# Performance work log

Hardware: AMD Instinct MI355X
Metric: run time of the kernel (lower is better)

## Reference

```python
import jax, jax.numpy as jnp
import numpy as np

B, N, D_MODEL, H, D_FF, NB_FEAT = 2, 2048, 512, 8, 2048, 256
DH = D_MODEL // H


def layer_norm(x, g, b, eps=1e-5):
    mu = jnp.mean(x, axis=-1, keepdims=True)
    var = jnp.mean((x - mu) ** 2, axis=-1, keepdims=True)
    return g * (x - mu) / jnp.sqrt(var + eps) + b


def softmax_kernel(data, proj, is_query, eps=1e-4):
    # Performer FAVOR+ positive random features. data: [b,h,n,dh], proj: [m,dh]
    dn = data.shape[-1] ** -0.25
    ratio = proj.shape[0] ** -0.5
    dd = jnp.einsum('bhnd,jd->bhnj', dn * data, proj)
    diag = (jnp.sum(data ** 2, axis=-1, keepdims=True) * 0.5) * (dn ** 2)
    if is_query:
        m = jnp.max(dd, axis=-1, keepdims=True)
    else:
        m = jnp.max(dd)
    return ratio * (jnp.exp(dd - diag - m) + eps)


def setup_inputs() -> dict:
    key = jax.random.key(0)
    ks = jax.random.split(key, 12)
    sd = D_MODEL ** -0.5
    sf = D_FF ** -0.5
    return {
        'x': jax.random.normal(ks[0], (B, N, D_MODEL), jnp.float32),
        'Wq': jax.random.normal(ks[1], (D_MODEL, D_MODEL), jnp.float32) * sd,
        'bq': jnp.zeros((D_MODEL,), jnp.float32),
        'Wk': jax.random.normal(ks[2], (D_MODEL, D_MODEL), jnp.float32) * sd,
        'bk': jnp.zeros((D_MODEL,), jnp.float32),
        'Wv': jax.random.normal(ks[3], (D_MODEL, D_MODEL), jnp.float32) * sd,
        'bv': jnp.zeros((D_MODEL,), jnp.float32),
        'Wo': jax.random.normal(ks[4], (D_MODEL, D_MODEL), jnp.float32) * sd,
        'bo': jnp.zeros((D_MODEL,), jnp.float32),
        'proj': jax.random.normal(ks[5], (NB_FEAT, DH), jnp.float32),
        'W1': jax.random.normal(ks[6], (D_MODEL, D_FF), jnp.float32) * sd,
        'b1': jnp.zeros((D_FF,), jnp.float32),
        'W2': jax.random.normal(ks[7], (D_FF, D_MODEL), jnp.float32) * sf,
        'b2': jnp.zeros((D_MODEL,), jnp.float32),
        'g1': jnp.ones((D_MODEL,), jnp.float32),
        'beta1': jnp.zeros((D_MODEL,), jnp.float32),
        'g2': jnp.ones((D_MODEL,), jnp.float32),
        'beta2': jnp.zeros((D_MODEL,), jnp.float32),
    }


def reference(x, Wq, bq, Wk, bk, Wv, bv, Wo, bo, proj, W1, b1, W2, b2, g1, beta1, g2, beta2):
    b, n, d = x.shape
    heads = lambda W, bias: (x @ W + bias).reshape(b, n, H, DH).transpose(0, 2, 1, 3)  # bhnd
    q = softmax_kernel(heads(Wq, bq), proj, is_query=True)   # [b,h,n,m]
    k = softmax_kernel(heads(Wk, bk), proj, is_query=False)  # [b,h,n,m]
    v = heads(Wv, bv)                                        # [b,h,n,dh]
    # non-causal linear attention
    k_sum = jnp.sum(k, axis=-2)                                   # [b,h,m]
    D_inv = 1.0 / jnp.einsum('bhnf,bhf->bhn', q, k_sum)           # [b,h,n]
    context = jnp.einsum('bhnf,bhne->bhfe', k, v)                 # [b,h,m,dh]
    out = jnp.einsum('bhfe,bhnf,bhn->bhne', context, q, D_inv)    # [b,h,n,dh]
    # output_attentions=True: effective attention matrix (abs, head-mean, detached)
    attn = jnp.einsum('bhnf,bhmf->bhnm', q, k) * D_inv[..., None]
    attn_weight = jax.lax.stop_gradient(jnp.mean(jnp.abs(attn), axis=1))  # [b,n,n]
    out = out.transpose(0, 2, 1, 3).reshape(b, n, d)
    out = out @ Wo + bo
    # NOTE: original module has no residual connections
    h1 = layer_norm(out, g1, beta1)
    ff = jax.nn.relu(h1 @ W1 + b1) @ W2 + b2
    y = layer_norm(ff, g2, beta2)
    return y, attn_weight
```

## Files before the change

kernel.cpp:

```cpp
#include <hip/hip_runtime.h>
#include <math.h>

#define B_SZ   2
#define N_TOK  2048
#define DM     512
#define NH     8
#define DHH    64
#define NF     256
#define DFF    2048
#define HF     2048
#define LDQKV  1536

constexpr float DN_SCALE   = 0.35355339059327373f;
constexpr float DIAG_SCALE = 0.0625f;
constexpr float RATIO      = 0.0625f;
constexpr float FEPS       = 1e-4f;
constexpr float LN_EPS     = 1e-5f;

typedef __attribute__((ext_vector_type(8))) short bf16x8;
typedef __attribute__((ext_vector_type(8))) _Float16 f16x8;
typedef __attribute__((ext_vector_type(4))) float f32x4;

__device__ __forceinline__ short f2b(float f) {
  union { float f; unsigned u; } x; x.f = f;
  unsigned r = (x.u + 0x7fff + ((x.u >> 16) & 1)) >> 16;
  return (short)r;
}
__device__ __forceinline__ float b2f(short s) {
  union { unsigned u; float f; } x; x.u = ((unsigned)(unsigned short)s) << 16;
  return x.f;
}
__device__ __forceinline__ void gload16(const void* g, void* l) {
  __builtin_amdgcn_global_load_lds((const __attribute__((address_space(1))) void*)g,
                                   (__attribute__((address_space(3))) void*)l, 16, 0, 0);
}
__device__ __forceinline__ int swz64(int row, int kbyte) {
  return (row * 128 + kbyte) ^ ((row & 7) << 4);
}

constexpr size_t OFF_S0    = 0;
constexpr size_t OFF_CTXP  = 0;
constexpr size_t OFF_QB    = 4194304;
constexpr size_t OFF_OUT2  = 0;
constexpr size_t OFF_FF1B  = 2097152;
constexpr size_t OFF_FF2   = 6291456;
constexpr size_t OFF_QFB   = 8388608;
constexpr size_t OFF_KB    = 12582912;
constexpr size_t OFF_QKV   = 16777216;
constexpr size_t OFF_AOB   = 20971520;
constexpr size_t OFF_H1B   = 22020096;
constexpr size_t OFF_WOT   = 23068672;
constexpr size_t OFF_W1T   = 23199744;
constexpr size_t OFF_W2T   = 23724032;
constexpr size_t OFF_KSUM  = 24248320;
constexpr size_t OFF_DINV  = 24252416;
constexpr size_t OFF_CTXT  = 24285184;
constexpr size_t OFF_BMAX  = 24416256;
constexpr size_t OFF_GMAX  = 24416768;
constexpr size_t OFF_ROWC  = 24416832;
constexpr size_t OFF_PART  = 24420928;
constexpr size_t OFF_VSUMP = 24552000;

template<bool RELU, bool OUT_BF16, int BMODE, bool SWZ>
__global__ __launch_bounds__(256)
void gemm_mfma(const short* __restrict__ A, const short* __restrict__ Bt,
               const float* __restrict__ bias, void* __restrict__ Cout,
               int M, int N, int K, size_t sA, size_t sB, size_t sC, int ldC) {
  __shared__ short As[128 * 64];
  __shared__ short Bs[128 * 64];
  int tid = threadIdx.x;
  int lane = tid & 63, wave = tid >> 6;
  int wm = wave >> 1, wn = wave & 1;
  int bx = blockIdx.x, by = blockIdx.y;
  if (SWZ) {
    int nwg = gridDim.x * gridDim.y;
    int flat = by * gridDim.x + bx;
    int swz = (flat & 7) * (nwg >> 3) + (flat >> 3);
    bx = swz % gridDim.x; by = swz / gridDim.x;
  }
  int bm = by * 128, bn = bx * 128;
  const short* Ab = A + (size_t)blockIdx.z * sA;
  const short* Bb = Bt + (size_t)blockIdx.z * sB;
  const float* rc = (BMODE == 2) ? (bias + (size_t)blockIdx.z * M) : bias;

  f32x4 acc[4][4] = {};
  int srow = tid >> 3;
  int scol = (tid & 7) * 8;

  for (int k0 = 0; k0 < K; k0 += 64) {
    #pragma unroll
    for (int c = 0; c < 4; ++c) {
      int r = c * 32 + srow;
      gload16(Ab + (size_t)(bm + r) * K + k0 + scol, As + c * 2048 + wave * 512);
      gload16(Bb + (size_t)(bn + r) * K + k0 + scol, Bs + c * 2048 + wave * 512);
    }
    __syncthreads();
    #pragma unroll
    for (int kk = 0; kk < 2; ++kk) {
      bf16x8 af[4], bf[4];
      int kq = kk * 32 + (lane >> 4) * 8;
      #pragma unroll
      for (int i = 0; i < 4; ++i)
        af[i] = *(const bf16x8*)&As[(wm * 64 + i * 16 + (lane & 15)) * 64 + kq];
      #pragma unroll
      for (int j = 0; j < 4; ++j)
        bf[j] = *(const bf16x8*)&Bs[(wn * 64 + j * 16 + (lane & 15)) * 64 + kq];
      #pragma unroll
      for (int i = 0; i < 4; ++i)
        #pragma unroll
        for (int j = 0; j < 4; ++j)
          acc[i][j] = __builtin_amdgcn_mfma_f32_16x16x32_bf16(af[i], bf[j], acc[i][j], 0, 0, 0);
    }
    __syncthreads();
  }

  int row0 = bm + wm * 64, col0 = bn + wn * 64;
  #pragma unroll
  for (int i = 0; i < 4; ++i) {
    #pragma unroll
    for (int j = 0; j < 4; ++j) {
      int col = col0 + j * 16 + (lane & 15);
      float bv = (BMODE == 1) ? rc[col] : 0.f;
      #pragma unroll
      for (int r = 0; r < 4; ++r) {
        int row = row0 + i * 16 + (lane >> 4) * 4 + r;
        float v = acc[i][j][r] + bv;
        if (BMODE == 2) v += rc[row];
        if (RELU) v = fmaxf(v, 0.f);
        size_t off = (size_t)blockIdx.z * sC + (size_t)row * ldC + col;
        if (OUT_BF16) ((short*)Cout)[off] = f2b(v);
        else          ((float*)Cout)[off] = v;
      }
    }
  }
}

template<bool RELU, bool OUT_BF16>
__global__ __launch_bounds__(256)
void gemm_bn64(const short* __restrict__ A, const short* __restrict__ Bt,
               const float* __restrict__ bias, void* __restrict__ Cout,
               int M, int N, int K) {
  __shared__ short As[128 * 64];
  __shared__ short Bs[64 * 64];
  int tid = threadIdx.x, lane = tid & 63, wave = tid >> 6;
  int bn = blockIdx.x * 64, bm = blockIdx.y * 128;
  int srow = tid >> 3, scol = (tid & 7) * 8;
  f32x4 acc[2][4] = {};
  for (int k0 = 0; k0 < K; k0 += 64) {
    #pragma unroll
    for (int c = 0; c < 4; ++c)
      gload16(A + (size_t)(bm + c * 32 + srow) * K + k0 + scol, As + c * 2048 + wave * 512);
    #pragma unroll
    for (int c = 0; c < 2; ++c)
      gload16(Bt + (size_t)(bn + c * 32 + srow) * K + k0 + scol, Bs + c * 2048 + wave * 512);
    __syncthreads();
    #pragma unroll
    for (int kk = 0; kk < 2; ++kk) {
      bf16x8 af[2], bf[4];
      int kq = kk * 32 + (lane >> 4) * 8;
      #pragma unroll
      for (int i = 0; i < 2; ++i)
        af[i] = *(const bf16x8*)&As[(wave * 32 + i * 16 + (lane & 15)) * 64 + kq];
      #pragma unroll
      for (int j = 0; j < 4; ++j)
        bf[j] = *(const bf16x8*)&Bs[(j * 16 + (lane & 15)) * 64 + kq];
      #pragma unroll
      for (int i = 0; i < 2; ++i)
        #pragma unroll
        for (int j = 0; j < 4; ++j)
          acc[i][j] = __builtin_amdgcn_mfma_f32_16x16x32_bf16(af[i], bf[j], acc[i][j], 0, 0, 0);
    }
    __syncthreads();
  }
  #pragma unroll
  for (int i = 0; i < 2; ++i) {
    #pragma unroll
    for (int j = 0; j < 4; ++j) {
      int col = bn + j * 16 + (lane & 15);
      float bv = bias[col];
      #pragma unroll
      for (int r = 0; r < 4; ++r) {
        int row = bm + wave * 32 + i * 16 + (lane >> 4) * 4 + r;
        float v = acc[i][j][r] + bv;
        if (RELU) v = fmaxf(v, 0.f);
        if (OUT_BF16) ((short*)Cout)[(size_t)row * N + col] = f2b(v);
        else          ((float*)Cout)[(size_t)row * N + col] = v;
      }
    }
  }
}

__global__ void prep_kernel(const float* __restrict__ x, short* __restrict__ xb,
                            const float* Wq, const float* Wk, const float* Wv, const float* Wo,
                            short* Wqt, short* Wkt, short* Wvt, short* Wot,
                            const float* W1, short* W1t, const float* W2, short* W2t) {
  __shared__ float t[64][65];
  int id = blockIdx.x, tid = threadIdx.x;
  if (id >= 768) {
    size_t base = ((size_t)(id - 768) * 256 + tid) * 8;
    #pragma unroll
    for (int u = 0; u < 8; ++u) xb[base + u] = f2b(x[base + u]);
    return;
  }
  const float* W; short* Wt; int K, N, bx, by;
  if (id < 256) {
    int z = id >> 6, sub = id & 63;
    W  = (z == 0) ? Wq : (z == 1) ? Wk : (z == 2) ? Wv : Wo;
    Wt = (z == 0) ? Wqt : (z == 1) ? Wkt : (z == 2) ? Wvt : Wot;
    K = 512; N = 512; bx = sub & 7; by = sub >> 3;
  } else if (id < 512) {
    int sub = id - 256;
    W = W1; Wt = W1t; K = 512; N = 2048; bx = sub & 31; by = sub >> 5;
  } else {
    int sub = id - 512;
    W = W2; Wt = W2t; K = 2048; N = 512; bx = sub & 7; by = sub >> 3;
  }
  int k0 = by * 64, n0 = bx * 64;
  int lx = tid & 63, ly = tid >> 6;
  for (int r = ly; r < 64; r += 4)
    t[r][lx] = W[(size_t)(k0 + r) * N + n0 + lx];
  __syncthreads();
  for (int r = ly; r < 64; r += 4)
    Wt[(size_t)(n0 + r) * K + k0 + lx] = f2b(t[lx][r]);
}

template<bool IS_QUERY>
__global__ __launch_bounds__(256)
void feat_mfma_kernel(const float* __restrict__ qkv, int coff, const float* __restrict__ bias,
                      const float* __restrict__ proj, short* __restrict__ qout,
                      float* __restrict__ part, float* __restrict__ bmax) {
  __shared__ short qh[64 * 64], ql[64 * 64];
  __shared__ short ph[128 * 64], pl[128 * 64];
  __shared__ float dpart[64][4];
  __shared__ float diag[64];
  __shared__ float wred[4];
  __shared__ float colp[4][256];
  int t = threadIdx.x;
  int bh = blockIdx.y, b = bh >> 3, h = bh & 7;
  int n0 = blockIdx.x * 64;
  int lane = t & 63, w = t >> 6, l15 = lane & 15, lq = lane >> 4;

  {
    int r = t >> 2, cg = (t & 3) * 16;
    const float* src = qkv + (size_t)(b * N_TOK + n0 + r) * LDQKV + coff + h * 64 + cg;
    const float* bs = bias + h * 64 + cg;
    float ss = 0.f;
    #pragma unroll
    for (int c2 = 0; c2 < 2; ++c2) {
      f16x8 H, L;
      #pragma unroll
      for (int u = 0; u < 8; ++u) {
        float xv = src[c2 * 8 + u] + bs[c2 * 8 + u];
        ss += xv * xv;
        _Float16 hi = (_Float16)xv;
        H[u] = hi;
        L[u] = (_Float16)(xv - (float)hi);
      }
      int off = swz64(r, cg * 2 + c2 * 16);
      *(f16x8*)((char*)qh + off) = H;
      *(f16x8*)((char*)ql + off) = L;
    }
    dpart[r][t & 3] = ss;
  }
  __syncthreads();
  if (t < 64)
    diag[t] = (dpart[t][0] + dpart[t][1] + dpart[t][2] + dpart[t][3]) * DIAG_SCALE;

  f16x8 ah[2], al[2];
  #pragma unroll
  for (int kk = 0; kk < 2; ++kk) {
    int off = swz64(w * 16 + l15, kk * 64 + lq * 16);
    ah[kk] = *(f16x8*)((char*)qh + off);
    al[kk] = *(f16x8*)((char*)ql + off);
  }

  f32x4 acc[16] = {};
  #pragma unroll
  for (int half = 0; half < 2; ++half) {
    __syncthreads();
    {
      int r = t & 127, cg = (t >> 7) * 32;
      const float* src = proj + (size_t)(half * 128 + r) * DHH + cg;
      #pragma unroll
      for (int c2 = 0; c2 < 4; ++c2) {
        f16x8 H, L;
        #pragma unroll
        for (int u = 0; u < 8; ++u) {
          float xv = src[c2 * 8 + u];
          _Float16 hi = (_Float16)xv;
          H[u] = hi;
          L[u] = (_Float16)(xv - (float)hi);
        }
        int off = swz64(r, cg * 2 + c2 * 16);
        *(f16x8*)((char*)ph + off) = H;
        *(f16x8*)((char*)pl + off) = L;
      }
    }
    __syncthreads();
    #pragma unroll
    for (int jl = 0; jl < 8; ++jl) {
      int row = jl * 16 + l15;
      #pragma unroll
      for (int kk = 0; kk < 2; ++kk) {
        int off = swz64(row, kk * 64 + lq * 16);
        f16x8 bh8 = *(f16x8*)((char*)ph + off);
        f16x8 bl8 = *(f16x8*)((char*)pl + off);
        acc[half * 8 + jl] = __builtin_amdgcn_mfma_f32_16x16x32_f16(ah[kk], bh8, acc[half * 8 + jl], 0, 0, 0);
        acc[half * 8 + jl] = __builtin_amdgcn_mfma_f32_16x16x32_f16(al[kk], bh8, acc[half * 8 + jl], 0, 0, 0);
        acc[half * 8 + jl] = __builtin_amdgcn_mfma_f32_16x16x32_f16(ah[kk], bl8, acc[half * 8 + jl], 0, 0, 0);
      }
    }
  }

  if (IS_QUERY) {
    #pragma unroll
    for (int r = 0; r < 4; ++r) {
      float mx = -3.4e38f;
      #pragma unroll
      for (int j = 0; j < 16; ++j) mx = fmaxf(mx, acc[j][r]);
      #pragma unroll
      for (int o = 1; o < 16; o <<= 1) mx = fmaxf(mx, __shfl_xor(mx, o, 64));
      int lrow = w * 16 + lq * 4 + r;
      float dg = diag[lrow];
      float ddm = mx * DN_SCALE;
      size_t base = (size_t)(b * N_TOK + n0 + lrow) * HF + h * NF + l15;
      #pragma unroll
      for (int j = 0; j < 16; ++j) {
        float v = RATIO * (expf(acc[j][r] * DN_SCALE - dg - ddm) + FEPS);
        qout[base + j * 16] = f2b(v);
      }
    }
  } else {
    float mxall = -3.4e38f;
    float cs[16];
    #pragma unroll
    for (int j = 0; j < 16; ++j) cs[j] = 0.f;
    #pragma unroll
    for (int r = 0; r < 4; ++r) {
      int lrow = w * 16 + lq * 4 + r;
      float dg = diag[lrow];
      size_t base = (size_t)(b * N_TOK + n0 + lrow) * HF + h * NF + l15;
      #pragma unroll
      for (int j = 0; j < 16; ++j) {
        float a = acc[j][r];
        mxall = fmaxf(mxall, a);
        float e = expf(a * DN_SCALE - dg);
        cs[j] += e;
        qout[base + j * 16] = f2b(e);
      }
    }
    #pragma unroll
    for (int j = 0; j < 16; ++j) {
      cs[j] += __shfl_xor(cs[j], 16, 64);
      cs[j] += __shfl_xor(cs[j], 32, 64);
    }
    if (lq == 0) {
      #pragma unroll
      for (int j = 0; j < 16; ++j) colp[w][j * 16 + l15] = cs[j];
    }
    #pragma unroll
    for (int o = 1; o < 64; o <<= 1) mxall = fmaxf(mxall, __shfl_xor(mxall, o, 64));
    if (lane == 0) wred[w] = mxall;
    __syncthreads();
    part[(size_t)(bh * 32 + blockIdx.x) * 256 + t] =
        colp[0][t] + colp[1][t] + colp[2][t] + colp[3][t];
    if (t == 0)
      bmax[bh * 32 + blockIdx.x] =
          fmaxf(fmaxf(wred[0], wred[1]), fmaxf(wred[2], wred[3])) * DN_SCALE;
  }
}

__global__ void ksum_final_kernel(const float* __restrict__ part, const float* __restrict__ bmax,
                                  float* __restrict__ ksum, float* __restrict__ gmax) {
  __shared__ float red[4];
  __shared__ float bc[1];
  int bh = blockIdx.x, t = threadIdx.x;
  float m = fmaxf(bmax[t], bmax[t + 256]);
  #pragma unroll
  for (int o = 1; o < 64; o <<= 1) m = fmaxf(m, __shfl_xor(m, o, 64));
  if ((t & 63) == 0) red[t >> 6] = m;
  __syncthreads();
  if (t == 0) {
    bc[0] = fmaxf(fmaxf(red[0], red[1]), fmaxf(red[2], red[3]));
    if (bh == 0) gmax[0] = bc[0];
  }
  __syncthreads();
  float s = expf(-bc[0]);
  float sum = 0.f;
  #pragma unroll 8
  for (int c = 0; c < 32; ++c) sum += part[(size_t)(bh * 32 + c) * 256 + t];
  ksum[bh * 256 + t] = RATIO * (s * sum + (float)N_TOK * FEPS);
}

__global__ __launch_bounds__(256)
void dinvqs_kernel(const short* __restrict__ qfb, const float* __restrict__ ksum,
                   const float* __restrict__ gmax, float* __restrict__ Dinv,
                   float* __restrict__ rowc, short* __restrict__ qb) {
  __shared__ float wsum[4];
  int R = blockIdx.x;
  int b = R >> 11, n = R & 2047;
  int t = threadIdx.x;
  float sc = RATIO * expf(-gmax[0]);
  bf16x8 qv = *(const bf16x8*)(qfb + (size_t)R * HF + t * 8);
  const float* ks = ksum + b * 2048 + t * 8;
  float p = 0.f;
  #pragma unroll
  for (int u = 0; u < 8; ++u) p += b2f(qv[u]) * ks[u];
  #pragma unroll
  for (int o = 1; o < 32; o <<= 1) p += __shfl_xor(p, o, 64);
  float d = 1.0f / p;
  if ((t & 31) == 0) Dinv[(b * NH + (t >> 5)) * N_TOK + n] = d;
  float dv = d * 0.125f;
  float qs = 0.f;
  bf16x8 o8;
  #pragma unroll
  for (int u = 0; u < 8; ++u) {
    float qb_f = b2f(qv[u]) * dv;
    qs += qb_f;
    o8[u] = f2b(qb_f * sc);
  }
  *(bf16x8*)(qb + (size_t)R * HF + t * 8) = o8;
  #pragma unroll
  for (int o = 1; o < 64; o <<= 1) qs += __shfl_xor(qs, o, 64);
  if ((t & 63) == 0) wsum[t >> 6] = qs;
  __syncthreads();
  if (t == 0) rowc[R] = RATIO * FEPS * (wsum[0] + wsum[1] + wsum[2] + wsum[3]);
}

__global__ __launch_bounds__(256)
void ctx_part_kernel(const short* __restrict__ kb, const float* __restrict__ qkv,
                     const float* __restrict__ bv, float* __restrict__ ctxp,
                     float* __restrict__ vsump) {
  int bh = blockIdx.y, b = bh >> 3, h = bh & 7;
  int f0 = blockIdx.x * 64;
  int ns = blockIdx.z * 256;
  __shared__ float kf[32][68];
  __shared__ float vs[32][68];
  int tid = threadIdx.x;
  int tf = (tid >> 4) * 4, te = (tid & 15) * 4;
  float acc[4][4] = {};
  float vloc[4] = {};
  for (int n0 = ns; n0 < ns + 256; n0 += 32) {
    #pragma unroll
    for (int i = 0; i < 8; i++) {
      int idx = tid + i * 256;
      int nn = idx >> 6, f = idx & 63;
      kf[nn][f] = b2f(kb[(size_t)(b * N_TOK + n0 + nn) * HF + h * NF + f0 + f]);
    }
    #pragma unroll
    for (int i = 0; i < 8; i++) {
      int idx = tid + i * 256;
      int nn = idx >> 6, e = idx & 63;
      vs[nn][e] = qkv[(size_t)(b * N_TOK + n0 + nn) * LDQKV + 1024 + h * DHH + e] + bv[h * DHH + e];
    }
    __syncthreads();
    #pragma unroll
    for (int nn = 0; nn < 32; nn++) {
      float a[4], bb[4];
      #pragma unroll
      for (int i = 0; i < 4; i++) a[i] = kf[nn][tf + i];
      #pragma unroll
      for (int j = 0; j < 4; j++) bb[j] = vs[nn][te + j];
      #pragma unroll
      for (int i = 0; i < 4; i++)
        #pragma unroll
        for (int j = 0; j < 4; j++) acc[i][j] += a[i] * bb[j];
    }
    if (blockIdx.x == 0 && (tid >> 4) == 0) {
      #pragma unroll
      for (int j = 0; j < 4; j++) {
        float s = 0.f;
        for (int nn = 0; nn < 32; nn++) s += vs[nn][te + j];
        vloc[j] += s;
      }
    }
    __syncthreads();
  }
  #pragma unroll
  for (int i = 0; i < 4; i++)
    #pragma unroll
    for (int j = 0; j < 4; j++)
      ctxp[(size_t)blockIdx.z * 262144 + (size_t)bh * 16384 +
           (size_t)(f0 + tf + i) * 64 + te + j] = acc[i][j];
  if (blockIdx.x == 0 && (tid >> 4) == 0) {
    #pragma unroll
    for (int j = 0; j < 4; j++)
      vsump[((size_t)blockIdx.z * 16 + bh) * 64 + te + j] = vloc[j];
  }
}

__global__ __launch_bounds__(256)
void ctx_reduce_kernel(const float* __restrict__ ctxp, const float* __restrict__ vsump,
                       const float* __restrict__ gmax, short* __restrict__ ctxT) {
  __shared__ float T[64][65];
  int ftile = blockIdx.x, bh = blockIdx.y;
  int tid = threadIdx.x;
  int e = tid & 63, q = tid >> 6;
  float s = expf(-gmax[0]);
  float vsum_e = 0.f;
  #pragma unroll
  for (int c = 0; c < 8; ++c) vsum_e += vsump[((size_t)c * 16 + bh) * 64 + e];
  #pragma unroll
  for (int i = 0; i < 16; ++i) {
    int fl = i * 4 + q;
    size_t idx = (size_t)bh * 16384 + (size_t)(ftile * 64 + fl) * 64 + e;
    float sum = 0.f;
    #pragma unroll
    for (int c = 0; c < 8; ++c) sum += ctxp[(size_t)c * 262144 + idx];
    T[fl][e] = RATIO * (s * sum + FEPS * vsum_e);
  }
  __syncthreads();
  #pragma unroll
  for (int i = 0; i < 16; ++i) {
    int er = i * 4 + q;
    ctxT[(size_t)bh * 16384 + (size_t)er * 256 + ftile * 64 + e] = f2b(T[e][er]);
  }
}

__global__ __launch_bounds__(256)
void pv_mfma_kernel(const short* __restrict__ qfb, const short* __restrict__ ctxT,
                    const float* __restrict__ Dinv, short* __restrict__ aob) {
  __shared__ short As[128 * 64];
  __shared__ short Bs[64 * 64];
  int bh = blockIdx.y, b = bh >> 3, h = bh & 7;
  int n0 = blockIdx.x * 128;
  int tid = threadIdx.x;
  int lane = tid & 63, wave = tid >> 6;
  int srow = tid >> 3, scol = (tid & 7) * 8;

  f32x4 acc[2][4] = {};
  for (int k0 = 0; k0 < NF; k0 += 64) {
    #pragma unroll
    for (int c = 0; c < 4; ++c) {
      int r = c * 32 + srow;
      gload16(qfb + (size_t)(b * N_TOK + n0 + r) * HF + h * NF + k0 + scol,
              As + c * 2048 + wave * 512);
    }
    #pragma unroll
    for (int c = 0; c < 2; ++c) {
      int r = c * 32 + srow;
      gload16(ctxT + (size_t)bh * 16384 + (size_t)r * 256 + k0 + scol,
              Bs + c * 2048 + wave * 512);
    }
    __syncthreads();
    #pragma unroll
    for (int kk = 0; kk < 2; ++kk) {
      bf16x8 af[2], bf[4];
      int kq = kk * 32 + (lane >> 4) * 8;
      #pragma unroll
      for (int i = 0; i < 2; ++i)
        af[i] = *(const bf16x8*)&As[(wave * 32 + i * 16 + (lane & 15)) * 64 + kq];
      #pragma unroll
      for (int j = 0; j < 4; ++j)
        bf[j] = *(const bf16x8*)&Bs[(j * 16 + (lane & 15)) * 64 + kq];
      #pragma unroll
      for (int i = 0; i < 2; ++i)
        #pragma unroll
        for (int j = 0; j < 4; ++j)
          acc[i][j] = __builtin_amdgcn_mfma_f32_16x16x32_bf16(af[i], bf[j], acc[i][j], 0, 0, 0);
    }
    __syncthreads();
  }

  #pragma unroll
  for (int i = 0; i < 2; ++i) {
    #pragma unroll
    for (int j = 0; j < 4; ++j) {
      int e = j * 16 + (lane & 15);
      #pragma unroll
      for (int r = 0; r < 4; ++r) {
        int n = n0 + wave * 32 + i * 16 + (lane >> 4) * 4 + r;
        float dv = Dinv[bh * N_TOK + n];
        aob[(size_t)(b * N_TOK + n) * DM + h * DHH + e] = f2b(acc[i][j][r] * dv);
      }
    }
  }
}

template<bool OUT_BF16>
__global__ void ln_kernel(const float* __restrict__ x, const float* __restrict__ g,
                          const float* __restrict__ beta, void* __restrict__ y) {
  int row = blockIdx.x, t = threadIdx.x;
  __shared__ float red[4];
  __shared__ float bcast[2];
  const float* xr = x + (size_t)row * DM;
  float v0 = xr[t], v1 = xr[t + 256];
  float s = v0 + v1;
  #pragma unroll
  for (int o = 32; o > 0; o >>= 1) s += __shfl_xor(s, o, 64);
  if ((t & 63) == 0) red[t >> 6] = s;
  __syncthreads();
  if (t == 0) bcast[0] = (red[0] + red[1] + red[2] + red[3]) * (1.0f / 512.0f);
  __syncthreads();
  float mean = bcast[0];
  float d0 = v0 - mean, d1 = v1 - mean;
  float s2 = d0 * d0 + d1 * d1;
  #pragma unroll
  for (int o = 32; o > 0; o >>= 1) s2 += __shfl_xor(s2, o, 64);
  if ((t & 63) == 0) red[t >> 6] = s2;
  __syncthreads();
  if (t == 0) bcast[1] = (red[0] + red[1] + red[2] + red[3]) * (1.0f / 512.0f);
  __syncthreads();
  float inv = rsqrtf(bcast[1] + LN_EPS);
  float o0 = g[t] * d0 * inv + beta[t];
  float o1 = g[t + 256] * d1 * inv + beta[t + 256];
  if (OUT_BF16) {
    ((short*)y)[(size_t)row * DM + t] = f2b(o0);
    ((short*)y)[(size_t)row * DM + t + 256] = f2b(o1);
  } else {
    ((float*)y)[(size_t)row * DM + t] = o0;
    ((float*)y)[(size_t)row * DM + t + 256] = o1;
  }
}

extern "C" void kernel_launch(void* const* d_in, const int* in_sizes, int n_in,
                              void* d_out, int out_size, void* d_ws, size_t ws_size,
                              hipStream_t stream) {
  const float* x     = (const float*)d_in[0];
  const float* Wq    = (const float*)d_in[1];
  const float* bq    = (const float*)d_in[2];
  const float* Wk    = (const float*)d_in[3];
  const float* bk    = (const float*)d_in[4];
  const float* Wv    = (const float*)d_in[5];
  const float* bv    = (const float*)d_in[6];
  const float* Wo    = (const float*)d_in[7];
  const float* bo    = (const float*)d_in[8];
  const float* proj  = (const float*)d_in[9];
  const float* W1    = (const float*)d_in[10];
  const float* b1    = (const float*)d_in[11];
  const float* W2    = (const float*)d_in[12];
  const float* b2    = (const float*)d_in[13];
  const float* g1    = (const float*)d_in[14];
  const float* beta1 = (const float*)d_in[15];
  const float* g2    = (const float*)d_in[16];
  const float* beta2 = (const float*)d_in[17];

  float* ws = (float*)d_ws;
  float* y_out = (float*)d_out;
  float* attnw = y_out + (size_t)B_SZ * N_TOK * DM;

  float* ctxp  = ws + OFF_CTXP;
  short* qb    = (short*)(ws + OFF_QB);
  float* out2  = ws + OFF_OUT2;
  short* ff1b  = (short*)(ws + OFF_FF1B);
  float* ff2   = ws + OFF_FF2;
  short* qfb   = (short*)(ws + OFF_QFB);
  short* xb    = (short*)(ws + OFF_QFB);
  short* kb    = (short*)(ws + OFF_KB);
  short* Wqkvt = (short*)(ws + OFF_KB);
  float* QKVlin = ws + OFF_QKV;
  short* aob   = (short*)(ws + OFF_AOB);
  short* h1b   = (short*)(ws + OFF_H1B);
  short* Wot   = (short*)(ws + OFF_WOT);
  short* W1t   = (short*)(ws + OFF_W1T);
  short* W2t   = (short*)(ws + OFF_W2T);
  float* ksum  = ws + OFF_KSUM;
  float* Dinv  = ws + OFF_DINV;
  short* ctxT  = (short*)(ws + OFF_CTXT);
  float* bmax  = ws + OFF_BMAX;
  float* gmax  = ws + OFF_GMAX;
  float* rowc  = ws + OFF_ROWC;
  float* part  = ws + OFF_PART;
  float* vsump = ws + OFF_VSUMP;

  dim3 blk(256);
  int MT = B_SZ * N_TOK;

  prep_kernel<<<1792, blk, 0, stream>>>(x, xb, Wq, Wk, Wv, Wo,
                                        Wqkvt, Wqkvt + 262144, Wqkvt + 524288, Wot,
                                        W1, W1t, W2, W2t);

  gemm_mfma<false, false, 0, false><<<dim3(LDQKV / 128, MT / 128, 1), blk, 0, stream>>>(
      xb, Wqkvt, nullptr, QKVlin, MT, LDQKV, DM, 0, 0, 0, LDQKV);

  feat_mfma_kernel<true><<<dim3(N_TOK / 64, B_SZ * NH), blk, 0, stream>>>(
      QKVlin, 0, bq, proj, qfb, nullptr, nullptr);
  feat_mfma_kernel<false><<<dim3(N_TOK / 64, B_SZ * NH), blk, 0, stream>>>(
      QKVlin, 512, bk, proj, kb, part, bmax);

  ksum_final_kernel<<<B_SZ * NH, blk, 0, stream>>>(part, bmax, ksum, gmax);
  dinvqs_kernel<<<MT, blk, 0, stream>>>(qfb, ksum, gmax, Dinv, rowc, qb);

  ctx_part_kernel<<<dim3(NF / 64, B_SZ * NH, 8), blk, 0, stream>>>(kb, QKVlin, bv, ctxp, vsump);
  ctx_reduce_kernel<<<dim3(4, B_SZ * NH), blk, 0, stream>>>(ctxp, vsump, gmax, ctxT);
  pv_mfma_kernel<<<dim3(N_TOK / 128, B_SZ * NH), blk, 0, stream>>>(qfb, ctxT, Dinv, aob);

  gemm_mfma<false, false, 2, true><<<dim3(16, 16, 2), blk, 0, stream>>>(
      qb, kb, rowc, attnw, N_TOK, N_TOK, HF,
      (size_t)N_TOK * HF, (size_t)N_TOK * HF, (size_t)N_TOK * N_TOK, N_TOK);

  gemm_bn64<false, false><<<dim3(DM / 64, MT / 128), blk, 0, stream>>>(
      aob, Wot, bo, out2, MT, DM, DM);

  ln_kernel<true><<<MT, blk, 0, stream>>>(out2, g1, beta1, h1b);
  gemm_mfma<true, true, 1, false><<<dim3(16, 32, 1), blk, 0, stream>>>(
      h1b, W1t, b1, ff1b, MT, DFF, DM, 0, 0, 0, DFF);
  gemm_bn64<false, false><<<dim3(DM / 64, MT / 128), blk, 0, stream>>>(
      ff1b, W2t, b2, ff2, MT, DM, DFF);
  ln_kernel<false><<<MT, blk, 0, stream>>>(ff2, g2, beta2, y_out);
}
```

Baseline: 263.6 us.

## Merge attention-stage kernels to cut launch count and fold global max reduction

The query and key feature kernels become one launch selected by blockIdx.z. The ksum and context-reduce kernels merge into one small kernel. The attention-weight GEMM and the PV GEMM share a single launch with block-index partitioning and a tiled block remap. The separate global-max write is gone, and each consumer block now recomputes the max from the 512 per-block maxima. This removes several launches and lets the small PV work overlap the large attention-weight GEMM, at the cost of redundant max reductions in every dinvqs block.

```diff
diff --git a/kernel.cpp b/kernel.cpp
--- a/kernel.cpp
+++ b/kernel.cpp
@@ -37,8 +37,19 @@
 __device__ __forceinline__ int swz64(int row, int kbyte) {
   return (row * 128 + kbyte) ^ ((row & 7) << 4);
 }
-
-constexpr size_t OFF_S0    = 0;
+__device__ __forceinline__ float reduce_bmax512(const float* __restrict__ bmax,
+                                                float* __restrict__ red) {
+  int t = threadIdx.x;
+  float m = fmaxf(bmax[t], bmax[t + 256]);
+  #pragma unroll
+  for (int o = 1; o < 64; o <<= 1) m = fmaxf(m, __shfl_xor(m, o, 64));
+  if ((t & 63) == 0) red[t >> 6] = m;
+  __syncthreads();
+  float r = fmaxf(fmaxf(red[0], red[1]), fmaxf(red[2], red[3]));
+  __syncthreads();
+  return r;
+}
+
 constexpr size_t OFF_CTXP  = 0;
 constexpr size_t OFF_QB    = 4194304;
 constexpr size_t OFF_OUT2  = 0;
@@ -56,32 +67,21 @@
 constexpr size_t OFF_DINV  = 24252416;
 constexpr size_t OFF_CTXT  = 24285184;
 constexpr size_t OFF_BMAX  = 24416256;
-constexpr size_t OFF_GMAX  = 24416768;
 constexpr size_t OFF_ROWC  = 24416832;
 constexpr size_t OFF_PART  = 24420928;
 constexpr size_t OFF_VSUMP = 24552000;
 
-template<bool RELU, bool OUT_BF16, int BMODE, bool SWZ>
+template<bool RELU, bool OUT_BF16, int BMODE>
 __global__ __launch_bounds__(256)
 void gemm_mfma(const short* __restrict__ A, const short* __restrict__ Bt,
                const float* __restrict__ bias, void* __restrict__ Cout,
-               int M, int N, int K, size_t sA, size_t sB, size_t sC, int ldC) {
+               int M, int N, int K, int ldC) {
   __shared__ short As[128 * 64];
   __shared__ short Bs[128 * 64];
   int tid = threadIdx.x;
   int lane = tid & 63, wave = tid >> 6;
   int wm = wave >> 1, wn = wave & 1;
-  int bx = blockIdx.x, by = blockIdx.y;
-  if (SWZ) {
-    int nwg = gridDim.x * gridDim.y;
-    int flat = by * gridDim.x + bx;
-    int swz = (flat & 7) * (nwg >> 3) + (flat >> 3);
-    bx = swz % gridDim.x; by = swz / gridDim.x;
-  }
-  int bm = by * 128, bn = bx * 128;
-  const short* Ab = A + (size_t)blockIdx.z * sA;
-  const short* Bb = Bt + (size_t)blockIdx.z * sB;
-  const float* rc = (BMODE == 2) ? (bias + (size_t)blockIdx.z * M) : bias;
+  int bm = blockIdx.y * 128, bn = blockIdx.x * 128;
 
   f32x4 acc[4][4] = {};
   int srow = tid >> 3;
@@ -91,8 +91,8 @@
     #pragma unroll
     for (int c = 0; c < 4; ++c) {
       int r = c * 32 + srow;
-      gload16(Ab + (size_t)(bm + r) * K + k0 + scol, As + c * 2048 + wave * 512);
-      gload16(Bb + (size_t)(bn + r) * K + k0 + scol, Bs + c * 2048 + wave * 512);
+      gload16(A + (size_t)(bm + r) * K + k0 + scol, As + c * 2048 + wave * 512);
+      gload16(Bt + (size_t)(bn + r) * K + k0 + scol, Bs + c * 2048 + wave * 512);
     }
     __syncthreads();
     #pragma unroll
@@ -120,14 +120,13 @@
     #pragma unroll
     for (int j = 0; j < 4; ++j) {
       int col = col0 + j * 16 + (lane & 15);
-      float bv = (BMODE == 1) ? rc[col] : 0.f;
+      float bv = (BMODE == 1) ? bias[col] : 0.f;
       #pragma unroll
       for (int r = 0; r < 4; ++r) {
         int row = row0 + i * 16 + (lane >> 4) * 4 + r;
         float v = acc[i][j][r] + bv;
-        if (BMODE == 2) v += rc[row];
         if (RELU) v = fmaxf(v, 0.f);
-        size_t off = (size_t)blockIdx.z * sC + (size_t)row * ldC + col;
+        size_t off = (size_t)row * ldC + col;
         if (OUT_BF16) ((short*)Cout)[off] = f2b(v);
         else          ((float*)Cout)[off] = v;
       }
@@ -224,10 +223,10 @@
     Wt[(size_t)(n0 + r) * K + k0 + lx] = f2b(t[lx][r]);
 }
 
-template<bool IS_QUERY>
 __global__ __launch_bounds__(256)
-void feat_mfma_kernel(const float* __restrict__ qkv, int coff, const float* __restrict__ bias,
-                      const float* __restrict__ proj, short* __restrict__ qout,
+void feat_mfma_kernel(const float* __restrict__ qkv, const float* __restrict__ bq,
+                      const float* __restrict__ bk, const float* __restrict__ proj,
+                      short* __restrict__ qfb, short* __restrict__ kbo,
                       float* __restrict__ part, float* __restrict__ bmax) {
   __shared__ short qh[64 * 64], ql[64 * 64];
   __shared__ short ph[128 * 64], pl[128 * 64];
@@ -236,6 +235,10 @@
   __shared__ float wred[4];
   __shared__ float colp[4][256];
   int t = threadIdx.x;
+  bool isq = (blockIdx.z == 0);
+  int coff = isq ? 0 : 512;
+  const float* bias = isq ? bq : bk;
+  short* qout = isq ? qfb : kbo;
   int bh = blockIdx.y, b = bh >> 3, h = bh & 7;
   int n0 = blockIdx.x * 64;
   int lane = t & 63, w = t >> 6, l15 = lane & 15, lq = lane >> 4;
@@ -312,7 +315,7 @@
     }
   }
 
-  if (IS_QUERY) {
+  if (isq) {
     #pragma unroll
     for (int r = 0; r < 4; ++r) {
       float mx = -3.4e38f;
@@ -368,63 +371,6 @@
       bmax[bh * 32 + blockIdx.x] =
           fmaxf(fmaxf(wred[0], wred[1]), fmaxf(wred[2], wred[3])) * DN_SCALE;
   }
-}
-
-__global__ void ksum_final_kernel(const float* __restrict__ part, const float* __restrict__ bmax,
-                                  float* __restrict__ ksum, float* __restrict__ gmax) {
-  __shared__ float red[4];
-  __shared__ float bc[1];
-  int bh = blockIdx.x, t = threadIdx.x;
-  float m = fmaxf(bmax[t], bmax[t + 256]);
-  #pragma unroll
-  for (int o = 1; o < 64; o <<= 1) m = fmaxf(m, __shfl_xor(m, o, 64));
-  if ((t & 63) == 0) red[t >> 6] = m;
-  __syncthreads();
-  if (t == 0) {
-    bc[0] = fmaxf(fmaxf(red[0], red[1]), fmaxf(red[2], red[3]));
-    if (bh == 0) gmax[0] = bc[0];
-  }
-  __syncthreads();
-  float s = expf(-bc[0]);
-  float sum = 0.f;
-  #pragma unroll 8
-  for (int c = 0; c < 32; ++c) sum += part[(size_t)(bh * 32 + c) * 256 + t];
-  ksum[bh * 256 + t] = RATIO * (s * sum + (float)N_TOK * FEPS);
-}
-
-__global__ __launch_bounds__(256)
-void dinvqs_kernel(const short* __restrict__ qfb, const float* __restrict__ ksum,
-                   const float* __restrict__ gmax, float* __restrict__ Dinv,
-                   float* __restrict__ rowc, short* __restrict__ qb) {
-  __shared__ float wsum[4];
-  int R = blockIdx.x;
-  int b = R >> 11, n = R & 2047;
-  int t = threadIdx.x;
-  float sc = RATIO * expf(-gmax[0]);
-  bf16x8 qv = *(const bf16x8*)(qfb + (size_t)R * HF + t * 8);
-  const float* ks = ksum + b * 2048 + t * 8;
-  float p = 0.f;
-  #pragma unroll
-  for (int u = 0; u < 8; ++u) p += b2f(qv[u]) * ks[u];
-  #pragma unroll
-  for (int o = 1; o < 32; o <<= 1) p += __shfl_xor(p, o, 64);
-  float d = 1.0f / p;
-  if ((t & 31) == 0) Dinv[(b * NH + (t >> 5)) * N_TOK + n] = d;
-  float dv = d * 0.125f;
-  float qs = 0.f;
-  bf16x8 o8;
-  #pragma unroll
-  for (int u = 0; u < 8; ++u) {
-    float qb_f = b2f(qv[u]) * dv;
-    qs += qb_f;
-    o8[u] = f2b(qb_f * sc);
-  }
-  *(bf16x8*)(qb + (size_t)R * HF + t * 8) = o8;
-  #pragma unroll
-  for (int o = 1; o < 64; o <<= 1) qs += __shfl_xor(qs, o, 64);
-  if ((t & 63) == 0) wsum[t >> 6] = qs;
-  __syncthreads();
-  if (t == 0) rowc[R] = RATIO * FEPS * (wsum[0] + wsum[1] + wsum[2] + wsum[3]);
 }
 
 __global__ __launch_bounds__(256)
@@ -490,88 +436,197 @@
 }
 
 __global__ __launch_bounds__(256)
-void ctx_reduce_kernel(const float* __restrict__ ctxp, const float* __restrict__ vsump,
-                       const float* __restrict__ gmax, short* __restrict__ ctxT) {
+void smallfat_kernel(const float* __restrict__ part, const float* __restrict__ bmax,
+                     float* __restrict__ ksum, const float* __restrict__ ctxp,
+                     const float* __restrict__ vsump, short* __restrict__ ctxT) {
   __shared__ float T[64][65];
-  int ftile = blockIdx.x, bh = blockIdx.y;
-  int tid = threadIdx.x;
-  int e = tid & 63, q = tid >> 6;
-  float s = expf(-gmax[0]);
-  float vsum_e = 0.f;
-  #pragma unroll
-  for (int c = 0; c < 8; ++c) vsum_e += vsump[((size_t)c * 16 + bh) * 64 + e];
-  #pragma unroll
-  for (int i = 0; i < 16; ++i) {
-    int fl = i * 4 + q;
-    size_t idx = (size_t)bh * 16384 + (size_t)(ftile * 64 + fl) * 64 + e;
+  __shared__ float red[4];
+  int t = threadIdx.x;
+  float m = reduce_bmax512(bmax, red);
+  float s = expf(-m);
+  if (blockIdx.x < 16) {
+    int bh = blockIdx.x;
     float sum = 0.f;
-    #pragma unroll
-    for (int c = 0; c < 8; ++c) sum += ctxp[(size_t)c * 262144 + idx];
-    T[fl][e] = RATIO * (s * sum + FEPS * vsum_e);
-  }
-  __syncthreads();
-  #pragma unroll
-  for (int i = 0; i < 16; ++i) {
-    int er = i * 4 + q;
-    ctxT[(size_t)bh * 16384 + (size_t)er * 256 + ftile * 64 + e] = f2b(T[e][er]);
+    #pragma unroll 8
+    for (int c = 0; c < 32; ++c) sum += part[(size_t)(bh * 32 + c) * 256 + t];
+    ksum[bh * 256 + t] = RATIO * (s * sum + (float)N_TOK * FEPS);
+  } else {
+    int id = blockIdx.x - 16;
+    int ftile = id & 3, bh = id >> 2;
+    int e = t & 63, q = t >> 6;
+    float vsum_e = 0.f;
+    #pragma unroll
+    for (int c = 0; c < 8; ++c) vsum_e += vsump[((size_t)c * 16 + bh) * 64 + e];
+    #pragma unroll
+    for (int i = 0; i < 16; ++i) {
+      int fl = i * 4 + q;
+      size_t idx = (size_t)bh * 16384 + (size_t)(ftile * 64 + fl) * 64 + e;
+      float sum = 0.f;
+      #pragma unroll
+      for (int c = 0; c < 8; ++c) sum += ctxp[(size_t)c * 262144 + idx];
+      T[fl][e] = RATIO * (s * sum + FEPS * vsum_e);
+    }
+    __syncthreads();
+    #pragma unroll
+    for (int i = 0; i < 16; ++i) {
+      int er = i * 4 + q;
+      ctxT[(size_t)bh * 16384 + (size_t)er * 256 + ftile * 64 + e] = f2b(T[e][er]);
+    }
   }
 }
 
 __global__ __launch_bounds__(256)
-void pv_mfma_kernel(const short* __restrict__ qfb, const short* __restrict__ ctxT,
-                    const float* __restrict__ Dinv, short* __restrict__ aob) {
+void dinvqs_kernel(const short* __restrict__ qfb, const float* __restrict__ ksum,
+                   const float* __restrict__ bmax, float* __restrict__ Dinv,
+                   float* __restrict__ rowc, short* __restrict__ qb) {
+  __shared__ float red[4];
+  __shared__ float wsum[4];
+  int R = blockIdx.x;
+  int b = R >> 11, n = R & 2047;
+  int t = threadIdx.x;
+  float m = reduce_bmax512(bmax, red);
+  float sc = RATIO * expf(-m);
+  bf16x8 qv = *(const bf16x8*)(qfb + (size_t)R * HF + t * 8);
+  const float* ks = ksum + b * 2048 + t * 8;
+  float p = 0.f;
+  #pragma unroll
+  for (int u = 0; u < 8; ++u) p += b2f(qv[u]) * ks[u];
+  #pragma unroll
+  for (int o = 1; o < 32; o <<= 1) p += __shfl_xor(p, o, 64);
+  float d = 1.0f / p;
+  if ((t & 31) == 0) Dinv[(b * NH + (t >> 5)) * N_TOK + n] = d;
+  float dv = d * 0.125f;
+  float qs = 0.f;
+  bf16x8 o8;
+  #pragma unroll
+  for (int u = 0; u < 8; ++u) {
+    float qb_f = b2f(qv[u]) * dv;
+    qs += qb_f;
+    o8[u] = f2b(qb_f * sc);
+  }
+  *(bf16x8*)(qb + (size_t)R * HF + t * 8) = o8;
+  #pragma unroll
+  for (int o = 1; o < 64; o <<= 1) qs += __shfl_xor(qs, o, 64);
+  if ((t & 63) == 0) wsum[t >> 6] = qs;
+  __syncthreads();
+  if (t == 0) rowc[R] = RATIO * FEPS * (wsum[0] + wsum[1] + wsum[2] + wsum[3]);
+}
+
+__global__ __launch_bounds__(256)
+void fat_attnw_pv(const short* __restrict__ qb, const short* __restrict__ kb,
+                  const float* __restrict__ rowc, float* __restrict__ attnw,
+                  const short* __restrict__ qfb, const short* __restrict__ ctxT,
+                  const float* __restrict__ Dinv, short* __restrict__ aob) {
   __shared__ short As[128 * 64];
-  __shared__ short Bs[64 * 64];
-  int bh = blockIdx.y, b = bh >> 3, h = bh & 7;
-  int n0 = blockIdx.x * 128;
+  __shared__ short Bs[128 * 64];
+  int bid = blockIdx.x;
   int tid = threadIdx.x;
   int lane = tid & 63, wave = tid >> 6;
   int srow = tid >> 3, scol = (tid & 7) * 8;
 
-  f32x4 acc[2][4] = {};
-  for (int k0 = 0; k0 < NF; k0 += 64) {
-    #pragma unroll
-    for (int c = 0; c < 4; ++c) {
-      int r = c * 32 + srow;
-      gload16(qfb + (size_t)(b * N_TOK + n0 + r) * HF + h * NF + k0 + scol,
-              As + c * 2048 + wave * 512);
-    }
-    #pragma unroll
-    for (int c = 0; c < 2; ++c) {
-      int r = c * 32 + srow;
-      gload16(ctxT + (size_t)bh * 16384 + (size_t)r * 256 + k0 + scol,
-              Bs + c * 2048 + wave * 512);
-    }
-    __syncthreads();
-    #pragma unroll
-    for (int kk = 0; kk < 2; ++kk) {
-      bf16x8 af[2], bf[4];
-      int kq = kk * 32 + (lane >> 4) * 8;
-      #pragma unroll
-      for (int i = 0; i < 2; ++i)
-        af[i] = *(const bf16x8*)&As[(wave * 32 + i * 16 + (lane & 15)) * 64 + kq];
-      #pragma unroll
-      for (int j = 0; j < 4; ++j)
-        bf[j] = *(const bf16x8*)&Bs[(j * 16 + (lane & 15)) * 64 + kq];
-      #pragma unroll
-      for (int i = 0; i < 2; ++i)
+  if (bid < 512) {
+    int z = bid >> 8;
+    int flat = bid & 255;
+    int tile = flat >> 4, wi = flat & 15;
+    int by = (tile >> 2) * 4 + (wi >> 2);
+    int bx = (tile & 3) * 4 + (wi & 3);
+    int bm = by * 128, bn = bx * 128;
+    const short* Ab = qb + (size_t)z * N_TOK * HF;
+    const short* Bb = kb + (size_t)z * N_TOK * HF;
+    const float* rc = rowc + (size_t)z * N_TOK;
+    float* out = attnw + (size_t)z * N_TOK * N_TOK;
+    int wm = wave >> 1, wn = wave & 1;
+
+    f32x4 acc[4][4] = {};
+    for (int k0 = 0; k0 < HF; k0 += 64) {
+      #pragma unroll
+      for (int c = 0; c < 4; ++c) {
+        int r = c * 32 + srow;
+        gload16(Ab + (size_t)(bm + r) * HF + k0 + scol, As + c * 2048 + wave * 512);
+        gload16(Bb + (size_t)(bn + r) * HF + k0 + scol, Bs + c * 2048 + wave * 512);
+      }
+      __syncthreads();
+      #pragma unroll
+      for (int kk = 0; kk < 2; ++kk) {
+        bf16x8 af[4], bf[4];
+        int kq = kk * 32 + (lane >> 4) * 8;
+        #pragma unroll
+        for (int i = 0; i < 4; ++i)
+          af[i] = *(const bf16x8*)&As[(wm * 64 + i * 16 + (lane & 15)) * 64 + kq];
         #pragma unroll
         for (int j = 0; j < 4; ++j)
-          acc[i][j] = __builtin_amdgcn_mfma_f32_16x16x32_bf16(af[i], bf[j], acc[i][j], 0, 0, 0);
-    }
-    __syncthreads();
-  }
-
-  #pragma unroll
-  for (int i = 0; i < 2; ++i) {
-    #pragma unroll
-    for (int j = 0; j < 4; ++j) {
-      int e = j * 16 + (lane & 15);
-      #pragma unroll
-      for (int r = 0; r < 4; ++r) {
-        int n = n0 + wave * 32 + i * 16 + (lane >> 4) * 4 + r;
-        float dv = Dinv[bh * N_TOK + n];
-        aob[(size_t)(b * N_TOK + n) * DM + h * DHH + e] = f2b(acc[i][j][r] * dv);
+          bf[j] = *(const bf16x8*)&Bs[(wn * 64 + j * 16 + (lane & 15)) * 64 + kq];
+        #pragma unroll
+        for (int i = 0; i < 4; ++i)
+          #pragma unroll
+          for (int j = 0; j < 4; ++j)
+            acc[i][j] = __builtin_amdgcn_mfma_f32_16x16x32_bf16(af[i], bf[j], acc[i][j], 0, 0, 0);
+      }
+      __syncthreads();
+    }
+    int row0 = bm + wm * 64, col0 = bn + wn * 64;
+    #pragma unroll
+    for (int i = 0; i < 4; ++i) {
+      #pragma unroll
+      for (int j = 0; j < 4; ++j) {
+        int col = col0 + j * 16 + (lane & 15);
+        #pragma unroll
+        for (int r = 0; r < 4; ++r) {
+          int row = row0 + i * 16 + (lane >> 4) * 4 + r;
+          out[(size_t)row * N_TOK + col] = acc[i][j][r] + rc[row];
+        }
+      }
+    }
+  } else {
+    int pid = bid - 512;
+    int bx = pid & 15, bh = pid >> 4;
+    int b = bh >> 3, h = bh & 7;
+    int n0 = bx * 128;
+
+    f32x4 acc[2][4] = {};
+    for (int k0 = 0; k0 < NF; k0 += 64) {
+      #pragma unroll
+      for (int c = 0; c < 4; ++c) {
+        int r = c * 32 + srow;
+        gload16(qfb + (size_t)(b * N_TOK + n0 + r) * HF + h * NF + k0 + scol,
+                As + c * 2048 + wave * 512);
+      }
+      #pragma unroll
+      for (int c = 0; c < 2; ++c) {
+        int r = c * 32 + srow;
+        gload16(ctxT + (size_t)bh * 16384 + (size_t)r * 256 + k0 + scol,
+                Bs + c * 2048 + wave * 512);
+      }
+      __syncthreads();
+      #pragma unroll
+      for (int kk = 0; kk < 2; ++kk) {
+        bf16x8 af[2], bf[4];
+        int kq = kk * 32 + (lane >> 4) * 8;
+        #pragma unroll
+        for (int i = 0; i < 2; ++i)
+          af[i] = *(const bf16x8*)&As[(wave * 32 + i * 16 + (lane & 15)) * 64 + kq];
+        #pragma unroll
+        for (int j = 0; j < 4; ++j)
+          bf[j] = *(const bf16x8*)&Bs[(j * 16 + (lane & 15)) * 64 + kq];
+        #pragma unroll
+        for (int i = 0; i < 2; ++i)
+          #pragma unroll
+          for (int j = 0; j < 4; ++j)
+            acc[i][j] = __builtin_amdgcn_mfma_f32_16x16x32_bf16(af[i], bf[j], acc[i][j], 0, 0, 0);
+      }
+      __syncthreads();
+    }
+    #pragma unroll
+    for (int i = 0; i < 2; ++i) {
+      #pragma unroll
+      for (int j = 0; j < 4; ++j) {
+        int e = j * 16 + (lane & 15);
+        #pragma unroll
+        for (int r = 0; r < 4; ++r) {
+          int n = n0 + wave * 32 + i * 16 + (lane >> 4) * 4 + r;
+          float dv = Dinv[bh * N_TOK + n];
+          aob[(size_t)(b * N_TOK + n) * DM + h * DHH + e] = f2b(acc[i][j][r] * dv);
+        }
       }
     }
   }
@@ -658,7 +713,6 @@
   float* Dinv  = ws + OFF_DINV;
   short* ctxT  = (short*)(ws + OFF_CTXT);
   float* bmax  = ws + OFF_BMAX;
-  float* gmax  = ws + OFF_GMAX;
   float* rowc  = ws + OFF_ROWC;
   float* part  = ws + OFF_PART;
   float* vsump = ws + OFF_VSUMP;
@@ -670,31 +724,26 @@
                                         Wqkvt, Wqkvt + 262144, Wqkvt + 524288, Wot,
                                         W1, W1t, W2, W2t);
 
-  gemm_mfma<false, false, 0, false><<<dim3(LDQKV / 128, MT / 128, 1), blk, 0, stream>>>(
-      xb, Wqkvt, nullptr, QKVlin, MT, LDQKV, DM, 0, 0, 0, LDQKV);
-
-  feat_mfma_kernel<true><<<dim3(N_TOK / 64, B_SZ * NH), blk, 0, stream>>>(
-      QKVlin, 0, bq, proj, qfb, nullptr, nullptr);
-  feat_mfma_kernel<false><<<dim3(N_TOK / 64, B_SZ * NH), blk, 0, stream>>>(
-      QKVlin, 512, bk, proj, kb, part, bmax);
-
-  ksum_final_kernel<<<B_SZ * NH, blk, 0, stream>>>(part, bmax, ksum, gmax);
-  dinvqs_kernel<<<MT, blk, 0, stream>>>(qfb, ksum, gmax, Dinv, rowc, qb);
+  gemm_mfma<false, false, 0><<<dim3(LDQKV / 128, MT / 128), blk, 0, stream>>>(
+      xb, Wqkvt, nullptr, QKVlin, MT, LDQKV, DM, LDQKV);
+
+  feat_mfma_kernel<<<dim3(N_TOK / 64, B_SZ * NH, 2), blk, 0, stream>>>(
+      QKVlin, bq, bk, proj, qfb, kb, part, bmax);
 
   ctx_part_kernel<<<dim3(NF / 64, B_SZ * NH, 8), blk, 0, stream>>>(kb, QKVlin, bv, ctxp, vsump);
-  ctx_reduce_kernel<<<dim3(4, B_SZ * NH), blk, 0, stream>>>(ctxp, vsump, gmax, ctxT);
-  pv_mfma_kernel<<<dim3(N_TOK / 128, B_SZ * NH), blk, 0, stream>>>(qfb, ctxT, Dinv, aob);
-
-  gemm_mfma<false, false, 2, true><<<dim3(16, 16, 2), blk, 0, stream>>>(
-      qb, kb, rowc, attnw, N_TOK, N_TOK, HF,
-      (size_t)N_TOK * HF, (size_t)N_TOK * HF, (size_t)N_TOK * N_TOK, N_TOK);
+
+  smallfat_kernel<<<80, blk, 0, stream>>>(part, bmax, ksum, ctxp, vsump, ctxT);
+
+  dinvqs_kernel<<<MT, blk, 0, stream>>>(qfb, ksum, bmax, Dinv, rowc, qb);
+
+  fat_attnw_pv<<<768, blk, 0, stream>>>(qb, kb, rowc, attnw, qfb, ctxT, Dinv, aob);
 
   gemm_bn64<false, false><<<dim3(DM / 64, MT / 128), blk, 0, stream>>>(
       aob, Wot, bo, out2, MT, DM, DM);
 
   ln_kernel<true><<<MT, blk, 0, stream>>>(out2, g1, beta1, h1b);
-  gemm_mfma<true, true, 1, false><<<dim3(16, 32, 1), blk, 0, stream>>>(
-      h1b, W1t, b1, ff1b, MT, DFF, DM, 0, 0, 0, DFF);
+  gemm_mfma<true, true, 1><<<dim3(DFF / 128, MT / 128), blk, 0, stream>>>(
+      h1b, W1t, b1, ff1b, MT, DFF, DM, DFF);
   gemm_bn64<false, false><<<dim3(DM / 64, MT / 128), blk, 0, stream>>>(
       ff1b, W2t, b2, ff2, MT, DM, DFF);
   ln_kernel<false><<<MT, blk, 0, stream>>>(ff2, g2, beta2, y_out);
```

New measurement: 250.1 us. -5.1%, faster.
